# Optimization experiments

Measured on AMD Instinct MI355X. Metric: run time of the kernel, lower is better.

The kernel has to match this reference:

```python
import jax, jax.numpy as jnp
import numpy as np

N_COG = 72  # 360 / delta_cog
N_RB = 72   # 360 / delta_rb
B, N, H = 64, 512, 128


def setup_inputs() -> dict:
    key = jax.random.key(0)
    k1, k2, k3, k4, k5, k6 = jax.random.split(key, 6)
    h_t = jax.random.normal(k1, (N, B, H), dtype=jnp.float32)
    r_mat = jax.random.randint(k2, (B, N, N), 0, N_RB, dtype=jnp.int32)
    d_mat = jax.random.uniform(k3, (B, N, N), dtype=jnp.float32)
    mask = jax.random.randint(k4, (B, N), 0, 2).astype(jnp.float32)
    cog_mat = jax.random.randint(k5, (B, N, N), 0, N_COG, dtype=jnp.int32)
    domain = jax.random.normal(k6, (N_COG, N_RB), dtype=jnp.float32)
    return {"h_t": h_t, "r_mat": r_mat, "d_mat": d_mat, "mask": mask,
            "cog_mat": cog_mat, "domain": domain}


def reference(h_t, r_mat, d_mat, mask, cog_mat, domain):
    # gather from learnable domain table, subtract distance, relu
    w = jax.nn.relu(domain[cog_mat, r_mat] - d_mat)          # [B, N, N]
    # pairwise mask (applied twice in the original, around normalization)
    m = mask[:, :, None] * mask[:, None, :]                   # [B, N, N]
    w = m * w
    # global-max normalize; torch uses .data.max() (no grad through max)
    w = w / jax.lax.stop_gradient(jnp.max(w))
    w = m * w
    # out[b,i,h] = sum_j w[b,i,j] * h_t[j,b,h]
    return jnp.einsum('bij,jbh->bih', w, h_t)                 # [B, N, H]
```

## Files before the change

kernel.cpp:

```cpp
#include <hip/hip_runtime.h>


#define B_   64
#define N_   512
#define H_   128
#define NCOG 72
#define NRB  72

typedef __bf16 bf16x8 __attribute__((ext_vector_type(8)));
typedef float  f32x4  __attribute__((ext_vector_type(4)));

__global__ __launch_bounds__(256) void k_transpose(const float* __restrict__ ht,
                                                   __bf16* __restrict__ T) {
    __shared__ __bf16 tile[32][136];
    const int jt = blockIdx.x * 32;
    const int b  = blockIdx.y;
    const int t  = threadIdx.x;
    {
        const int jj = t >> 3;
        const int h0 = (t & 7) << 4;
        const float* src = ht + ((size_t)(jt + jj) * B_ + b) * H_ + h0;
        float4 v0 = *(const float4*)(src + 0);
        float4 v1 = *(const float4*)(src + 4);
        float4 v2 = *(const float4*)(src + 8);
        float4 v3 = *(const float4*)(src + 12);
        __bf16* dst = &tile[jj][h0];
        dst[0]=(__bf16)v0.x; dst[1]=(__bf16)v0.y; dst[2]=(__bf16)v0.z; dst[3]=(__bf16)v0.w;
        dst[4]=(__bf16)v1.x; dst[5]=(__bf16)v1.y; dst[6]=(__bf16)v1.z; dst[7]=(__bf16)v1.w;
        dst[8]=(__bf16)v2.x; dst[9]=(__bf16)v2.y; dst[10]=(__bf16)v2.z; dst[11]=(__bf16)v2.w;
        dst[12]=(__bf16)v3.x; dst[13]=(__bf16)v3.y; dst[14]=(__bf16)v3.z; dst[15]=(__bf16)v3.w;
    }
    __syncthreads();
    {
        const int h  = t >> 1;
        const int j0 = (t & 1) << 4;
        union { bf16x8 v[2]; __bf16 e[16]; } ob;
        #pragma unroll
        for (int q = 0; q < 16; ++q) ob.e[q] = tile[j0 + q][h];
        __bf16* dst = T + ((size_t)b * H_ + h) * N_ + jt + j0;
        *(bf16x8*)(dst + 0) = ob.v[0];
        *(bf16x8*)(dst + 8) = ob.v[1];
    }
}

__global__ __launch_bounds__(256) void k_main(const int* __restrict__ cog,
                                              const int* __restrict__ rmat,
                                              const float* __restrict__ dmat,
                                              const float* __restrict__ mask,
                                              const float* __restrict__ domain,
                                              const __bf16* __restrict__ T,
                                              float* __restrict__ out,
                                              unsigned int* __restrict__ gmax) {
    __shared__ float sdom[NCOG * NRB];
    __shared__ float smask[N_];
    const int b  = blockIdx.y;
    const int i0 = blockIdx.x * 64;
    const int t  = threadIdx.x;
    for (int k = t; k < NCOG * NRB; k += 256) sdom[k] = domain[k];
    for (int k = t; k < N_; k += 256) smask[k] = mask[b * N_ + k];
    __syncthreads();

    const int wave = t >> 6;
    const int lane = t & 63;
    const int quad = lane >> 4;
    const int lrow = lane & 15;
    const int irow = i0 + wave * 16 + lrow;
    const size_t rowbase = ((size_t)b * N_ + irow) * N_;
    const float mi = smask[irow];
    const __bf16* Tb = T + (size_t)b * H_ * N_ + (size_t)lrow * N_;

    f32x4 acc[8];
    #pragma unroll
    for (int i = 0; i < 8; ++i) acc[i] = (f32x4)0.0f;
    float wmax = 0.0f;

    for (int kk = 0; kk < N_; kk += 32) {
        const int jb = kk + quad * 8;
        union { int4 v[2]; int e[8]; } ci, ri;
        union { float4 v[2]; float e[8]; } di, mj8;
        ci.v[0] = *(const int4*)(cog + rowbase + jb);
        ci.v[1] = *(const int4*)(cog + rowbase + jb + 4);
        ri.v[0] = *(const int4*)(rmat + rowbase + jb);
        ri.v[1] = *(const int4*)(rmat + rowbase + jb + 4);
        di.v[0] = *(const float4*)(dmat + rowbase + jb);
        di.v[1] = *(const float4*)(dmat + rowbase + jb + 4);
        mj8.v[0] = *(const float4*)(&smask[jb]);
        mj8.v[1] = *(const float4*)(&smask[jb + 4]);

        union { bf16x8 v8; __bf16 e[8]; } af;
        #pragma unroll
        for (int q = 0; q < 8; ++q) {
            float val = sdom[ci.e[q] * NRB + ri.e[q]] - di.e[q];
            val = fmaxf(val, 0.0f) * mj8.e[q];
            wmax = fmaxf(wmax, val);
            af.e[q] = (__bf16)val;
        }

        const __bf16* tb = Tb + kk + quad * 8;
        #pragma unroll
        for (int nt = 0; nt < 8; ++nt) {
            bf16x8 bf = *(const bf16x8*)(tb + (size_t)nt * 16 * N_);
            acc[nt] = __builtin_amdgcn_mfma_f32_16x16x32_bf16(af.v8, bf, acc[nt], 0, 0, 0);
        }
    }
    wmax *= mi;

    #pragma unroll
    for (int off = 32; off > 0; off >>= 1)
        wmax = fmaxf(wmax, __shfl_down(wmax, off));
    if (lane == 0) atomicMax(gmax, __float_as_uint(wmax));

    const int orow0 = i0 + wave * 16 + quad * 4;
    #pragma unroll
    for (int nt = 0; nt < 8; ++nt) {
        #pragma unroll
        for (int r = 0; r < 4; ++r)
            out[((size_t)b * N_ + orow0 + r) * H_ + nt * 16 + lrow] = acc[nt][r];
    }
}

__global__ __launch_bounds__(256) void k_scale(float* __restrict__ out,
                                               const float* __restrict__ mask,
                                               const unsigned int* __restrict__ gmax) {
    const float inv = 1.0f / __uint_as_float(*gmax);
    const int idx = blockIdx.x * 256 + threadIdx.x;
    const float m = mask[idx >> 5] * inv;
    float4* p = (float4*)out;
    float4 v = p[idx];
    v.x *= m; v.y *= m; v.z *= m; v.w *= m;
    p[idx] = v;
}

extern "C" void kernel_launch(void* const* d_in, const int* in_sizes, int n_in,
                              void* d_out, int out_size, void* d_ws, size_t ws_size,
                              hipStream_t stream) {
    const float* ht     = (const float*)d_in[0];
    const int*   rmat   = (const int*)  d_in[1];
    const float* dmat   = (const float*)d_in[2];
    const float* mask   = (const float*)d_in[3];
    const int*   cog    = (const int*)  d_in[4];
    const float* domain = (const float*)d_in[5];
    float* out = (float*)d_out;

    unsigned int* gmax = (unsigned int*)d_ws;
    __bf16* T = (__bf16*)((char*)d_ws + 256);

    hipMemsetAsync(d_ws, 0, 256, stream);
    k_transpose<<<dim3(16, 64), 256, 0, stream>>>(ht, T);
    k_main<<<dim3(8, 64), 256, 0, stream>>>(cog, rmat, dmat, mask, domain, T, out, gmax);
    k_scale<<<4096, 256, 0, stream>>>(out, mask, gmax);
}
```

Baseline: 269.3 us.

## Split K across two wave groups with LDS reduction and register prefetch

Doubles the block to 512 threads so two groups of four waves each handle half of the j-dimension, then sums their partial accumulators through shared memory before writing the output. The K loop is fully unrolled, and the next chunk of cog/rmat/dmat is prefetched into registers while the current chunk is computed. The per-wave atomicMax becomes a single per-block atomic. The aim is more waves in flight to hide memory latency on the streaming index/distance loads, at the cost of extra LDS (about 34KB for the reduction buffer), a block barrier, and higher register pressure.

Measured after the change: 251.2 us. 6.7% less time.

```diff
diff --git a/kernel.cpp b/kernel.cpp
--- a/kernel.cpp
+++ b/kernel.cpp
@@ -43,79 +43,116 @@
     }
 }
 
-__global__ __launch_bounds__(256) void k_main(const int* __restrict__ cog,
-                                              const int* __restrict__ rmat,
-                                              const float* __restrict__ dmat,
-                                              const float* __restrict__ mask,
-                                              const float* __restrict__ domain,
-                                              const __bf16* __restrict__ T,
-                                              float* __restrict__ out,
-                                              unsigned int* __restrict__ gmax) {
+struct Batch { int4 c0, c1, r0, r1; float4 d0, d1; };
+
+__global__ __launch_bounds__(512, 4) void k_main(const int* __restrict__ cog,
+                                                 const int* __restrict__ rmat,
+                                                 const float* __restrict__ dmat,
+                                                 const float* __restrict__ mask,
+                                                 const float* __restrict__ domain,
+                                                 const __bf16* __restrict__ T,
+                                                 float* __restrict__ out,
+                                                 unsigned int* __restrict__ gmax) {
     __shared__ float sdom[NCOG * NRB];
     __shared__ float smask[N_];
+    __shared__ float sred[4][16][132];
+    __shared__ float swmax[8];
     const int b  = blockIdx.y;
     const int i0 = blockIdx.x * 64;
     const int t  = threadIdx.x;
-    for (int k = t; k < NCOG * NRB; k += 256) sdom[k] = domain[k];
-    for (int k = t; k < N_; k += 256) smask[k] = mask[b * N_ + k];
+    for (int k = t; k < NCOG * NRB; k += 512) sdom[k] = domain[k];
+    for (int k = t; k < N_; k += 512) smask[k] = mask[b * N_ + k];
     __syncthreads();
 
     const int wave = t >> 6;
     const int lane = t & 63;
     const int quad = lane >> 4;
     const int lrow = lane & 15;
-    const int irow = i0 + wave * 16 + lrow;
+    const int wi   = wave & 3;
+    const int kh   = wave >> 2;
+    const int irow = i0 + wi * 16 + lrow;
     const size_t rowbase = ((size_t)b * N_ + irow) * N_;
-    const float mi = smask[irow];
-    const __bf16* Tb = T + (size_t)b * H_ * N_ + (size_t)lrow * N_;
+    const int kbeg = kh * 256;
+
+    const int*   cp = cog  + rowbase + kbeg + quad * 8;
+    const int*   rp = rmat + rowbase + kbeg + quad * 8;
+    const float* dp = dmat + rowbase + kbeg + quad * 8;
+    const __bf16* Tb = T + (size_t)b * H_ * N_ + (size_t)lrow * N_ + kbeg + quad * 8;
 
     f32x4 acc[8];
     #pragma unroll
     for (int i = 0; i < 8; ++i) acc[i] = (f32x4)0.0f;
     float wmax = 0.0f;
 
-    for (int kk = 0; kk < N_; kk += 32) {
-        const int jb = kk + quad * 8;
+    Batch cur, nxt;
+    cur.c0 = *(const int4*)(cp);     cur.c1 = *(const int4*)(cp + 4);
+    cur.r0 = *(const int4*)(rp);     cur.r1 = *(const int4*)(rp + 4);
+    cur.d0 = *(const float4*)(dp);   cur.d1 = *(const float4*)(dp + 4);
+
+    #pragma unroll
+    for (int s = 0; s < 8; ++s) {
+        const int kk = s * 32;
+        bf16x8 bf[8];
+        #pragma unroll
+        for (int nt = 0; nt < 8; ++nt)
+            bf[nt] = *(const bf16x8*)(Tb + kk + (size_t)nt * 16 * N_);
+        if (s < 7) {
+            nxt.c0 = *(const int4*)(cp + kk + 32);  nxt.c1 = *(const int4*)(cp + kk + 36);
+            nxt.r0 = *(const int4*)(rp + kk + 32);  nxt.r1 = *(const int4*)(rp + kk + 36);
+            nxt.d0 = *(const float4*)(dp + kk + 32); nxt.d1 = *(const float4*)(dp + kk + 36);
+        }
         union { int4 v[2]; int e[8]; } ci, ri;
-        union { float4 v[2]; float e[8]; } di, mj8;
-        ci.v[0] = *(const int4*)(cog + rowbase + jb);
-        ci.v[1] = *(const int4*)(cog + rowbase + jb + 4);
-        ri.v[0] = *(const int4*)(rmat + rowbase + jb);
-        ri.v[1] = *(const int4*)(rmat + rowbase + jb + 4);
-        di.v[0] = *(const float4*)(dmat + rowbase + jb);
-        di.v[1] = *(const float4*)(dmat + rowbase + jb + 4);
-        mj8.v[0] = *(const float4*)(&smask[jb]);
-        mj8.v[1] = *(const float4*)(&smask[jb + 4]);
-
+        union { float4 v[2]; float e[8]; } di;
+        ci.v[0] = cur.c0; ci.v[1] = cur.c1;
+        ri.v[0] = cur.r0; ri.v[1] = cur.r1;
+        di.v[0] = cur.d0; di.v[1] = cur.d1;
+        const int jb = kbeg + kk + quad * 8;
         union { bf16x8 v8; __bf16 e[8]; } af;
         #pragma unroll
         for (int q = 0; q < 8; ++q) {
             float val = sdom[ci.e[q] * NRB + ri.e[q]] - di.e[q];
-            val = fmaxf(val, 0.0f) * mj8.e[q];
+            val = fmaxf(val, 0.0f) * smask[jb + q];
             wmax = fmaxf(wmax, val);
             af.e[q] = (__bf16)val;
         }
-
-        const __bf16* tb = Tb + kk + quad * 8;
         #pragma unroll
-        for (int nt = 0; nt < 8; ++nt) {
-            bf16x8 bf = *(const bf16x8*)(tb + (size_t)nt * 16 * N_);
-            acc[nt] = __builtin_amdgcn_mfma_f32_16x16x32_bf16(af.v8, bf, acc[nt], 0, 0, 0);
-        }
+        for (int nt = 0; nt < 8; ++nt)
+            acc[nt] = __builtin_amdgcn_mfma_f32_16x16x32_bf16(af.v8, bf[nt], acc[nt], 0, 0, 0);
+        cur = nxt;
     }
-    wmax *= mi;
+    wmax *= smask[irow];
 
     #pragma unroll
     for (int off = 32; off > 0; off >>= 1)
         wmax = fmaxf(wmax, __shfl_down(wmax, off));
-    if (lane == 0) atomicMax(gmax, __float_as_uint(wmax));
+    if (lane == 0) swmax[wave] = wmax;
 
-    const int orow0 = i0 + wave * 16 + quad * 4;
-    #pragma unroll
-    for (int nt = 0; nt < 8; ++nt) {
+    if (kh == 1) {
         #pragma unroll
-        for (int r = 0; r < 4; ++r)
-            out[((size_t)b * N_ + orow0 + r) * H_ + nt * 16 + lrow] = acc[nt][r];
+        for (int nt = 0; nt < 8; ++nt)
+            #pragma unroll
+            for (int r = 0; r < 4; ++r)
+                sred[wi][quad * 4 + r][nt * 16 + lrow] = acc[nt][r];
+    }
+    __syncthreads();
+
+    if (t == 0) {
+        float m = swmax[0];
+        #pragma unroll
+        for (int w = 1; w < 8; ++w) m = fmaxf(m, swmax[w]);
+        atomicMax(gmax, __float_as_uint(m));
+    }
+
+    if (kh == 0) {
+        const int orow0 = i0 + wi * 16 + quad * 4;
+        #pragma unroll
+        for (int nt = 0; nt < 8; ++nt) {
+            #pragma unroll
+            for (int r = 0; r < 4; ++r) {
+                float v = acc[nt][r] + sred[wi][quad * 4 + r][nt * 16 + lrow];
+                out[((size_t)b * N_ + orow0 + r) * H_ + nt * 16 + lrow] = v;
+            }
+        }
     }
 }
 
@@ -147,6 +184,6 @@
 
     hipMemsetAsync(d_ws, 0, 256, stream);
     k_transpose<<<dim3(16, 64), 256, 0, stream>>>(ht, T);
-    k_main<<<dim3(8, 64), 256, 0, stream>>>(cog, rmat, dmat, mask, domain, T, out, gmax);
+    k_main<<<dim3(8, 64), 512, 0, stream>>>(cog, rmat, dmat, mask, domain, T, out, gmax);
     k_scale<<<4096, 256, 0, stream>>>(out, mask, gmax);
 }
```

## Double-buffer cog/rmat/dmat and T tiles through LDS with 512-thread blocks

Applied to the files above, without the earlier changes.

Restructures the main kernel into 512-thread blocks of 128 rows that stage the index, distance and transposed-feature tiles into swizzled, double-buffered shared memory. Global loads for the next step are issued ahead of the current compute so that memory latency overlaps the MFMA work. The block-to-batch mapping is also remapped, and the per-wave atomic max becomes one atomic per block. In exchange the kernel uses much more LDS (one block per CU), so occupancy drops and the code depends on hand-placed barriers.

Result: slower. 277.6 us (+3.1%).

```diff
diff --git a/kernel.cpp b/kernel.cpp
--- a/kernel.cpp
+++ b/kernel.cpp
@@ -43,72 +43,132 @@
     }
 }
 
-__global__ __launch_bounds__(256) void k_main(const int* __restrict__ cog,
-                                              const int* __restrict__ rmat,
-                                              const float* __restrict__ dmat,
-                                              const float* __restrict__ mask,
-                                              const float* __restrict__ domain,
-                                              const __bf16* __restrict__ T,
-                                              float* __restrict__ out,
-                                              unsigned int* __restrict__ gmax) {
-    __shared__ float sdom[NCOG * NRB];
-    __shared__ float smask[N_];
-    const int b  = blockIdx.y;
-    const int i0 = blockIdx.x * 64;
-    const int t  = threadIdx.x;
-    for (int k = t; k < NCOG * NRB; k += 256) sdom[k] = domain[k];
-    for (int k = t; k < N_; k += 256) smask[k] = mask[b * N_ + k];
-    __syncthreads();
-
-    const int wave = t >> 6;
-    const int lane = t & 63;
-    const int quad = lane >> 4;
-    const int lrow = lane & 15;
-    const int irow = i0 + wave * 16 + lrow;
-    const size_t rowbase = ((size_t)b * N_ + irow) * N_;
-    const float mi = smask[irow];
-    const __bf16* Tb = T + (size_t)b * H_ * N_ + (size_t)lrow * N_;
+__global__ __launch_bounds__(512, 1) void k_main(const int* __restrict__ cog,
+                                                 const int* __restrict__ rmat,
+                                                 const float* __restrict__ dmat,
+                                                 const float* __restrict__ mask,
+                                                 const float* __restrict__ domain,
+                                                 const __bf16* __restrict__ T,
+                                                 float* __restrict__ out,
+                                                 unsigned int* __restrict__ gmax) {
+    __shared__ int    wt[2][3][4096];
+    __shared__ __bf16 tt[2][H_][32];
+    __shared__ float  sdom[NCOG * NRB];
+    __shared__ float  smask[N_];
+    __shared__ float  swmax[8];
+
+    const int id = blockIdx.x;
+    const int b  = (id & 7) + 8 * (id >> 5);
+    const int i0 = ((id >> 3) & 3) * 128;
+
+    const int t = threadIdx.x, wave = t >> 6, lane = t & 63;
+
+    for (int k = t; k < NCOG * NRB; k += 512) sdom[k] = domain[k];
+    for (int k = t; k < N_; k += 512) smask[k] = mask[b * N_ + k];
+
+    const size_t robase = ((size_t)b * N_ + i0) * N_;
+
+    const int l8 = lane >> 3, l7 = lane & 7;
+    const int* gw[6];
+    int        wo[6];
+    #pragma unroll
+    for (int q = 0; q < 6; ++q) {
+        const int m = wave + 8 * q, a = m >> 4, sub = m & 15;
+        const int row = sub * 8 + l8;
+        const int* base = (a == 0) ? cog : (a == 1) ? rmat : (const int*)dmat;
+        gw[q] = base + robase + (size_t)row * N_ + l7 * 4;
+        wo[q] = a * 4096 + row * 32 + ((l7 ^ l8) * 4);
+    }
+    const __bf16* gT = T + (size_t)b * H_ * N_
+                         + (size_t)(wave * 16 + (lane >> 2)) * N_ + (lane & 3) * 8;
+    __bf16* ttw0 = &tt[0][wave * 16 + (lane >> 2)][(lane & 3) * 8];
+    __bf16* ttw1 = &tt[1][wave * 16 + (lane >> 2)][(lane & 3) * 8];
+
+    int4 ldw[2][6]; int4 ldt[2];
+
+    #define ISSUE(n, par) do {                                                  \
+        const int kk_ = (n) * 32;                                               \
+        _Pragma("unroll")                                                       \
+        for (int q = 0; q < 6; ++q) ldw[par][q] = *(const int4*)(gw[q] + kk_);  \
+        ldt[par] = *(const int4*)(gT + kk_); } while (0)
+
+    #define STAGE(par) do {                                                     \
+        int* wb = &wt[par][0][0];                                               \
+        _Pragma("unroll")                                                       \
+        for (int q = 0; q < 6; ++q) *(int4*)(wb + wo[q]) = ldw[par][q];         \
+        *(int4*)((par) ? ttw1 : ttw0) = ldt[par]; } while (0)
+
+    const int quad = lane >> 4, lrow = lane & 15;
+    const int row  = wave * 16 + lrow;
+    const int g0   = row * 32 + (((quad * 2) ^ (lrow & 7)) * 4);
+    const int g1   = g0 ^ 4;
 
     f32x4 acc[8];
     #pragma unroll
     for (int i = 0; i < 8; ++i) acc[i] = (f32x4)0.0f;
     float wmax = 0.0f;
 
-    for (int kk = 0; kk < N_; kk += 32) {
-        const int jb = kk + quad * 8;
-        union { int4 v[2]; int e[8]; } ci, ri;
-        union { float4 v[2]; float e[8]; } di, mj8;
-        ci.v[0] = *(const int4*)(cog + rowbase + jb);
-        ci.v[1] = *(const int4*)(cog + rowbase + jb + 4);
-        ri.v[0] = *(const int4*)(rmat + rowbase + jb);
-        ri.v[1] = *(const int4*)(rmat + rowbase + jb + 4);
-        di.v[0] = *(const float4*)(dmat + rowbase + jb);
-        di.v[1] = *(const float4*)(dmat + rowbase + jb + 4);
-        mj8.v[0] = *(const float4*)(&smask[jb]);
-        mj8.v[1] = *(const float4*)(&smask[jb + 4]);
-
-        union { bf16x8 v8; __bf16 e[8]; } af;
-        #pragma unroll
-        for (int q = 0; q < 8; ++q) {
-            float val = sdom[ci.e[q] * NRB + ri.e[q]] - di.e[q];
-            val = fmaxf(val, 0.0f) * mj8.e[q];
-            wmax = fmaxf(wmax, val);
-            af.e[q] = (__bf16)val;
-        }
-
-        const __bf16* tb = Tb + kk + quad * 8;
-        #pragma unroll
-        for (int nt = 0; nt < 8; ++nt) {
-            bf16x8 bf = *(const bf16x8*)(tb + (size_t)nt * 16 * N_);
-            acc[nt] = __builtin_amdgcn_mfma_f32_16x16x32_bf16(af.v8, bf, acc[nt], 0, 0, 0);
-        }
-    }
-    wmax *= mi;
+    #define COMPUTE(s, par) do {                                                \
+        const int jb = (s) * 32 + quad * 8;                                     \
+        const int* wp = &wt[par][0][0];                                         \
+        union { int4 v[2]; int   e[8]; } ci, ri;                                \
+        union { int4 v[2]; float e[8]; } di;                                    \
+        ci.v[0] = *(const int4*)(wp + g0);        ci.v[1] = *(const int4*)(wp + g1);        \
+        ri.v[0] = *(const int4*)(wp + 4096 + g0); ri.v[1] = *(const int4*)(wp + 4096 + g1); \
+        di.v[0] = *(const int4*)(wp + 8192 + g0); di.v[1] = *(const int4*)(wp + 8192 + g1); \
+        bf16x8 bf[8];                                                           \
+        _Pragma("unroll")                                                       \
+        for (int nt = 0; nt < 8; ++nt)                                          \
+            bf[nt] = *(const bf16x8*)&tt[par][nt * 16 + lrow][quad * 8];        \
+        union { bf16x8 v8; __bf16 e[8]; } af;                                   \
+        _Pragma("unroll")                                                       \
+        for (int q = 0; q < 8; ++q) {                                           \
+            float val = sdom[ci.e[q] * NRB + ri.e[q]] - di.e[q];                \
+            val = fmaxf(val, 0.0f) * smask[jb + q];                             \
+            wmax = fmaxf(wmax, val);                                            \
+            af.e[q] = (__bf16)val;                                              \
+        }                                                                       \
+        _Pragma("unroll")                                                       \
+        for (int nt = 0; nt < 8; ++nt)                                          \
+            acc[nt] = __builtin_amdgcn_mfma_f32_16x16x32_bf16(af.v8, bf[nt], acc[nt], 0, 0, 0); \
+    } while (0)
+
+    #define LBAR asm volatile("s_waitcnt lgkmcnt(0)\n\ts_barrier" ::: "memory")
+
+    ISSUE(0, 0);
+    ISSUE(1, 1);
+    STAGE(0);
+    LBAR;
+
+    for (int sp = 0; sp < 8; ++sp) {
+        const int s0 = sp * 2, s1 = s0 + 1;
+        if (s0 < 14) ISSUE(s0 + 2, 0);
+        STAGE(1);
+        COMPUTE(s0, 0);
+        LBAR;
+        if (s1 < 14) ISSUE(s1 + 2, 1);
+        if (s1 < 15) STAGE(0);
+        COMPUTE(s1, 1);
+        LBAR;
+    }
+    #undef ISSUE
+    #undef STAGE
+    #undef COMPUTE
+    #undef LBAR
+
+    wmax *= smask[i0 + row];
 
     #pragma unroll
     for (int off = 32; off > 0; off >>= 1)
         wmax = fmaxf(wmax, __shfl_down(wmax, off));
-    if (lane == 0) atomicMax(gmax, __float_as_uint(wmax));
+    if (lane == 0) swmax[wave] = wmax;
+    __syncthreads();
+    if (t == 0) {
+        float m = swmax[0];
+        #pragma unroll
+        for (int w = 1; w < 8; ++w) m = fmaxf(m, swmax[w]);
+        atomicMax(gmax, __float_as_uint(m));
+    }
 
     const int orow0 = i0 + wave * 16 + quad * 4;
     #pragma unroll
@@ -147,6 +207,6 @@
 
     hipMemsetAsync(d_ws, 0, 256, stream);
     k_transpose<<<dim3(16, 64), 256, 0, stream>>>(ht, T);
-    k_main<<<dim3(8, 64), 256, 0, stream>>>(cog, rmat, dmat, mask, domain, T, out, gmax);
+    k_main<<<dim3(256), 512, 0, stream>>>(cog, rmat, dmat, mask, domain, T, out, gmax);
     k_scale<<<4096, 256, 0, stream>>>(out, mask, gmax);
 }
```

## Split fused gather-GEMM into weight prepack kernel and tiled bf16 GEMM kernel

Applied to the files above, without the earlier changes.

Replaces the fused kernel that built the weight matrix and ran MFMA in the same loop with two kernels. The first gathers domain values, applies the mask and writes bf16 weights in a 32-column tiled layout, reducing the max per block before one atomic. The second runs a 512-thread GEMM over contiguous tiles with double-buffered register loads. The transposed h_t is also stored in matching 32-wide tiles. The split separates the latency-bound gather from the MFMA loop and gives more blocks for the gather, at the cost of an extra 32 MB bf16 round trip through global memory.

Result: faster. 255.1 us (-5.3%).

```diff
diff --git a/kernel.cpp b/kernel.cpp
--- a/kernel.cpp
+++ b/kernel.cpp
@@ -37,80 +37,131 @@
         union { bf16x8 v[2]; __bf16 e[16]; } ob;
         #pragma unroll
         for (int q = 0; q < 16; ++q) ob.e[q] = tile[j0 + q][h];
-        __bf16* dst = T + ((size_t)b * H_ + h) * N_ + jt + j0;
+        __bf16* dst = T + ((size_t)b * 16 + blockIdx.x) * 4096 + h * 32 + j0;
         *(bf16x8*)(dst + 0) = ob.v[0];
         *(bf16x8*)(dst + 8) = ob.v[1];
     }
 }
 
-__global__ __launch_bounds__(256) void k_main(const int* __restrict__ cog,
-                                              const int* __restrict__ rmat,
-                                              const float* __restrict__ dmat,
-                                              const float* __restrict__ mask,
-                                              const float* __restrict__ domain,
-                                              const __bf16* __restrict__ T,
-                                              float* __restrict__ out,
-                                              unsigned int* __restrict__ gmax) {
+__global__ __launch_bounds__(256) void k_prepack(const int* __restrict__ cog,
+                                                 const int* __restrict__ rmat,
+                                                 const float* __restrict__ dmat,
+                                                 const float* __restrict__ mask,
+                                                 const float* __restrict__ domain,
+                                                 __bf16* __restrict__ W,
+                                                 unsigned int* __restrict__ gmax) {
     __shared__ float sdom[NCOG * NRB];
     __shared__ float smask[N_];
+    __shared__ float swmax[4];
     const int b  = blockIdx.y;
-    const int i0 = blockIdx.x * 64;
+    const int i0 = blockIdx.x * 16;
     const int t  = threadIdx.x;
     for (int k = t; k < NCOG * NRB; k += 256) sdom[k] = domain[k];
     for (int k = t; k < N_; k += 256) smask[k] = mask[b * N_ + k];
     __syncthreads();
 
-    const int wave = t >> 6;
-    const int lane = t & 63;
-    const int quad = lane >> 4;
-    const int lrow = lane & 15;
-    const int irow = i0 + wave * 16 + lrow;
-    const size_t rowbase = ((size_t)b * N_ + irow) * N_;
-    const float mi = smask[irow];
-    const __bf16* Tb = T + (size_t)b * H_ * N_ + (size_t)lrow * N_;
-
-    f32x4 acc[8];
-    #pragma unroll
-    for (int i = 0; i < 8; ++i) acc[i] = (f32x4)0.0f;
+    const size_t base = ((size_t)b * N_ + i0) * N_;
     float wmax = 0.0f;
 
-    for (int kk = 0; kk < N_; kk += 32) {
-        const int jb = kk + quad * 8;
-        union { int4 v[2]; int e[8]; } ci, ri;
-        union { float4 v[2]; float e[8]; } di, mj8;
-        ci.v[0] = *(const int4*)(cog + rowbase + jb);
-        ci.v[1] = *(const int4*)(cog + rowbase + jb + 4);
-        ri.v[0] = *(const int4*)(rmat + rowbase + jb);
-        ri.v[1] = *(const int4*)(rmat + rowbase + jb + 4);
-        di.v[0] = *(const float4*)(dmat + rowbase + jb);
-        di.v[1] = *(const float4*)(dmat + rowbase + jb + 4);
-        mj8.v[0] = *(const float4*)(&smask[jb]);
-        mj8.v[1] = *(const float4*)(&smask[jb + 4]);
-
-        union { bf16x8 v8; __bf16 e[8]; } af;
+    #pragma unroll
+    for (int p = 0; p < 4; ++p) {
+        const int e  = p * 2048 + t * 8;
+        const int rl = e >> 9;
+        const int j  = e & 511;
+        const size_t off = base + (size_t)rl * N_ + j;
+        union { int4 v[2]; int   e8[8]; } ci, ri;
+        union { int4 v[2]; float f[8]; } di;
+        ci.v[0] = *(const int4*)(cog + off);   ci.v[1] = *(const int4*)(cog + off + 4);
+        ri.v[0] = *(const int4*)(rmat + off);  ri.v[1] = *(const int4*)(rmat + off + 4);
+        di.v[0] = *(const int4*)((const int*)dmat + off);
+        di.v[1] = *(const int4*)((const int*)dmat + off + 4);
+
+        union { bf16x8 v8; __bf16 h[8]; } wv;
+        float lmax = 0.0f;
         #pragma unroll
         for (int q = 0; q < 8; ++q) {
-            float val = sdom[ci.e[q] * NRB + ri.e[q]] - di.e[q];
-            val = fmaxf(val, 0.0f) * mj8.e[q];
-            wmax = fmaxf(wmax, val);
-            af.e[q] = (__bf16)val;
+            float val = sdom[ci.e8[q] * NRB + ri.e8[q]] - di.f[q];
+            val = fmaxf(val, 0.0f) * smask[j + q];
+            lmax = fmaxf(lmax, val);
+            wv.h[q] = (__bf16)val;
         }
-
-        const __bf16* tb = Tb + kk + quad * 8;
-        #pragma unroll
-        for (int nt = 0; nt < 8; ++nt) {
-            bf16x8 bf = *(const bf16x8*)(tb + (size_t)nt * 16 * N_);
-            acc[nt] = __builtin_amdgcn_mfma_f32_16x16x32_bf16(af.v8, bf, acc[nt], 0, 0, 0);
-        }
-    }
-    wmax *= mi;
+        wmax = fmaxf(wmax, lmax * smask[i0 + rl]);
+
+        const int i = i0 + rl;
+        __bf16* dst = W + ((size_t)(b * 4 + (i >> 7)) * 16 + (j >> 5)) * 4096
+                        + (i & 127) * 32 + (j & 31);
+        *(bf16x8*)dst = wv.v8;
+    }
 
     #pragma unroll
     for (int off = 32; off > 0; off >>= 1)
         wmax = fmaxf(wmax, __shfl_down(wmax, off));
-    if (lane == 0) atomicMax(gmax, __float_as_uint(wmax));
-
-    const int orow0 = i0 + wave * 16 + quad * 4;
+    if ((t & 63) == 0) swmax[t >> 6] = wmax;
+    __syncthreads();
+    if (t == 0) {
+        float m = fmaxf(fmaxf(swmax[0], swmax[1]), fmaxf(swmax[2], swmax[3]));
+        atomicMax(gmax, __float_as_uint(m));
+    }
+}
+
+__global__ __launch_bounds__(512, 1) void k_gemm(const __bf16* __restrict__ W,
+                                                 const __bf16* __restrict__ T,
+                                                 float* __restrict__ out) {
+    const int id = blockIdx.x;
+    const int b  = (id & 7) + 8 * (id >> 5);
+    const int it = (id >> 3) & 3;
+    const int t = threadIdx.x, wave = t >> 6, lane = t & 63;
+    const int quad = lane >> 4, lrow = lane & 15;
+
+    const __bf16* Ab = W + (size_t)(b * 4 + it) * 16 * 4096
+                         + (wave * 16 + lrow) * 32 + quad * 8;
+    const __bf16* Bb = T + (size_t)b * 16 * 4096 + lrow * 32 + quad * 8;
+
+    union U { int4 i; bf16x8 h; };
+    U av, bv0, bv1, bv2, bv3, bv4, bv5, bv6, bv7;
+    U au, bu0, bu1, bu2, bu3, bu4, bu5, bu6, bu7;
+
+    f32x4 acc[8];
+    #pragma unroll
+    for (int i = 0; i < 8; ++i) acc[i] = (f32x4)0.0f;
+
+    #define GLD(s, A, B0,B1,B2,B3,B4,B5,B6,B7) do {        \
+        const __bf16* ap = Ab + (s) * 4096;                 \
+        const __bf16* bp = Bb + (s) * 4096;                 \
+        A.i  = *(const int4*)ap;                            \
+        B0.i = *(const int4*)(bp + 0 * 512);                \
+        B1.i = *(const int4*)(bp + 1 * 512);                \
+        B2.i = *(const int4*)(bp + 2 * 512);                \
+        B3.i = *(const int4*)(bp + 3 * 512);                \
+        B4.i = *(const int4*)(bp + 4 * 512);                \
+        B5.i = *(const int4*)(bp + 5 * 512);                \
+        B6.i = *(const int4*)(bp + 6 * 512);                \
+        B7.i = *(const int4*)(bp + 7 * 512); } while (0)
+
+    #define COMP(A, B0,B1,B2,B3,B4,B5,B6,B7) do {                               \
+        acc[0] = __builtin_amdgcn_mfma_f32_16x16x32_bf16(A.h, B0.h, acc[0], 0, 0, 0); \
+        acc[1] = __builtin_amdgcn_mfma_f32_16x16x32_bf16(A.h, B1.h, acc[1], 0, 0, 0); \
+        acc[2] = __builtin_amdgcn_mfma_f32_16x16x32_bf16(A.h, B2.h, acc[2], 0, 0, 0); \
+        acc[3] = __builtin_amdgcn_mfma_f32_16x16x32_bf16(A.h, B3.h, acc[3], 0, 0, 0); \
+        acc[4] = __builtin_amdgcn_mfma_f32_16x16x32_bf16(A.h, B4.h, acc[4], 0, 0, 0); \
+        acc[5] = __builtin_amdgcn_mfma_f32_16x16x32_bf16(A.h, B5.h, acc[5], 0, 0, 0); \
+        acc[6] = __builtin_amdgcn_mfma_f32_16x16x32_bf16(A.h, B6.h, acc[6], 0, 0, 0); \
+        acc[7] = __builtin_amdgcn_mfma_f32_16x16x32_bf16(A.h, B7.h, acc[7], 0, 0, 0); \
+    } while (0)
+
+    GLD(0, av, bv0, bv1, bv2, bv3, bv4, bv5, bv6, bv7);
+    GLD(1, au, bu0, bu1, bu2, bu3, bu4, bu5, bu6, bu7);
+    for (int sp = 0; sp < 8; ++sp) {
+        const int s0 = sp * 2;
+        COMP(av, bv0, bv1, bv2, bv3, bv4, bv5, bv6, bv7);
+        if (s0 + 2 < 16) GLD(s0 + 2, av, bv0, bv1, bv2, bv3, bv4, bv5, bv6, bv7);
+        COMP(au, bu0, bu1, bu2, bu3, bu4, bu5, bu6, bu7);
+        if (s0 + 3 < 16) GLD(s0 + 3, au, bu0, bu1, bu2, bu3, bu4, bu5, bu6, bu7);
+    }
+    #undef GLD
+    #undef COMP
+
+    const int orow0 = it * 128 + wave * 16 + quad * 4;
     #pragma unroll
     for (int nt = 0; nt < 8; ++nt) {
         #pragma unroll
@@ -144,9 +195,11 @@
 
     unsigned int* gmax = (unsigned int*)d_ws;
     __bf16* T = (__bf16*)((char*)d_ws + 256);
+    __bf16* W = (__bf16*)((char*)d_ws + 256 + 8 * 1024 * 1024);
 
     hipMemsetAsync(d_ws, 0, 256, stream);
     k_transpose<<<dim3(16, 64), 256, 0, stream>>>(ht, T);
-    k_main<<<dim3(8, 64), 256, 0, stream>>>(cog, rmat, dmat, mask, domain, T, out, gmax);
+    k_prepack<<<dim3(32, 64), 256, 0, stream>>>(cog, rmat, dmat, mask, domain, W, gmax);
+    k_gemm<<<dim3(256), 512, 0, stream>>>(W, T, out);
     k_scale<<<4096, 256, 0, stream>>>(out, mask, gmax);
 }
```
